# Kernel optimization log

Hardware: AMD Instinct MI355X
Metric: run time of the kernel (lower is better)

Reference implementation:

```python
import jax, jax.numpy as jnp
import numpy as np
import math

B, T, C = 8, 2048, 1024
N_LAYER, LAYER_ID = 24, 12


def setup_inputs() -> dict:
    key = jax.random.key(0)
    ks = jax.random.split(key, 8)
    # deterministic parameter init, mirroring RWKV_TimeMix.__init__
    ratio_0_to_1 = LAYER_ID / (N_LAYER - 1)
    ratio_1_to_almost0 = 1.0 - LAYER_ID / N_LAYER
    h = np.arange(C, dtype=np.float64)
    time_decay = (-5 + 8 * (h / (C - 1)) ** (0.7 + 1.3 * ratio_0_to_1)).astype(np.float32)
    zigzag = (np.array([(i + 1) % 3 - 1 for i in range(C)], dtype=np.float64) * 0.5)
    time_first = (np.ones(C) * math.log(0.3) + zigzag).astype(np.float32)
    xpos = (np.arange(C, dtype=np.float64) / C)
    time_mix_k = (xpos ** ratio_1_to_almost0).astype(np.float32).reshape(1, 1, C)
    time_mix_v = (xpos ** ratio_1_to_almost0 + 0.3 * ratio_0_to_1).astype(np.float32).reshape(1, 1, C)
    time_mix_r = (xpos ** (0.5 * ratio_1_to_almost0)).astype(np.float32).reshape(1, 1, C)
    scale = 1.0 / math.sqrt(C)
    return {
        "x": jax.random.normal(ks[0], (B, T, C), jnp.float32),
        "time_decay": jnp.asarray(time_decay),
        "time_first": jnp.asarray(time_first),
        "time_mix_k": jnp.asarray(time_mix_k),
        "time_mix_v": jnp.asarray(time_mix_v),
        "time_mix_r": jnp.asarray(time_mix_r),
        "Wk": jax.random.normal(ks[1], (C, C), jnp.float32) * scale,
        "Wv": jax.random.normal(ks[2], (C, C), jnp.float32) * scale,
        "Wr": jax.random.normal(ks[3], (C, C), jnp.float32) * scale,
        "Wo": jax.random.normal(ks[4], (C, C), jnp.float32) * scale,
    }


def wkv_scan(w_decay, u, k, v):
    """Numerically-stable RWKV-4 WKV recurrence.
    w_decay, u: [C]; k, v: [B, T, C]. Returns [B, T, C].
    """
    w = -jnp.exp(w_decay)  # negative decay per channel
    kt = jnp.swapaxes(k, 0, 1)  # [T, B, C]
    vt = jnp.swapaxes(v, 0, 1)
    Bn, Cn = k.shape[0], k.shape[2]
    aa0 = jnp.zeros((Bn, Cn), k.dtype)
    bb0 = jnp.zeros((Bn, Cn), k.dtype)
    pp0 = jnp.full((Bn, Cn), -1e38, k.dtype)

    def step(carry, kv):
        aa, bb, pp = carry
        k_t, v_t = kv
        ww = u + k_t
        q = jnp.maximum(pp, ww)
        e1 = jnp.exp(pp - q)
        e2 = jnp.exp(ww - q)
        y = (e1 * aa + e2 * v_t) / (e1 * bb + e2)
        ww2 = pp + w
        q2 = jnp.maximum(ww2, k_t)
        e1 = jnp.exp(ww2 - q2)
        e2 = jnp.exp(k_t - q2)
        return (e1 * aa + e2 * v_t, e1 * bb + e2, q2), y

    _, ys = jax.lax.scan(step, (aa0, bb0, pp0), (kt, vt))
    return jnp.swapaxes(ys, 0, 1)  # [B, T, C]


def reference(x, time_decay, time_first, time_mix_k, time_mix_v, time_mix_r, Wk, Wv, Wr, Wo):
    # time shift: x_{t-1}, zero at t=0
    xx = jnp.pad(x, ((0, 0), (1, 0), (0, 0)))[:, :-1]
    xk = x * time_mix_k + xx * (1.0 - time_mix_k)
    xv = x * time_mix_v + xx * (1.0 - time_mix_v)
    xr = x * time_mix_r + xx * (1.0 - time_mix_r)
    k = jnp.einsum("btc,oc->bto", xk, Wk)
    v = jnp.einsum("btc,oc->bto", xv, Wv)
    r = jnp.einsum("btc,oc->bto", xr, Wr)
    wkv = wkv_scan(time_decay, time_first, k, v)
    rwkv = jax.nn.sigmoid(r) * wkv
    return jnp.einsum("btc,oc->bto", rwkv, Wo)
```

## Files before the change

kernel.cpp:

```cpp
#include <hip/hip_runtime.h>

#define BB 8
#define TT 2048
#define CC 1024
#define WKV_L 64
#define WKV_NCH (TT / WKV_L)

typedef __bf16 bf16x8_t __attribute__((ext_vector_type(8)));
typedef float f32x4_t __attribute__((ext_vector_type(4)));

__device__ __forceinline__ unsigned short f2bf(float f) {
  unsigned u = __float_as_uint(f);
  u += 0x7fffu + ((u >> 16) & 1u);
  return (unsigned short)(u >> 16);
}
__device__ __forceinline__ float bf2f(unsigned short s) {
  return __uint_as_float(((unsigned)s) << 16);
}

#define GLOAD16(gp, lp)                                                        \
  __builtin_amdgcn_global_load_lds(                                            \
      (const __attribute__((address_space(1))) void*)(gp),                     \
      (__attribute__((address_space(3))) void*)(lp), 16, 0, 0)

__global__ __launch_bounds__(256) void mix3_cast_kernel(
    const float* __restrict__ x, const float* __restrict__ tmk,
    const float* __restrict__ tmv, const float* __restrict__ tmr,
    unsigned short* __restrict__ xk, unsigned short* __restrict__ xv,
    unsigned short* __restrict__ xr) {
  const size_t total4 = (size_t)BB * TT * CC / 4;
  for (size_t i = (size_t)blockIdx.x * blockDim.x + threadIdx.x; i < total4;
       i += (size_t)gridDim.x * blockDim.x) {
    size_t e = i * 4;
    int c = (int)(e & (CC - 1));
    int t = (int)((e / CC) & (TT - 1));
    float4 xv4 = ((const float4*)x)[i];
    float4 xp = make_float4(0.f, 0.f, 0.f, 0.f);
    if (t > 0) xp = ((const float4*)x)[i - CC / 4];
    float4 mk = *(const float4*)(tmk + c);
    float4 mv = *(const float4*)(tmv + c);
    float4 mr = *(const float4*)(tmr + c);
    ushort4 ok, ov, orr;
    ok.x = f2bf(xv4.x * mk.x + xp.x * (1.f - mk.x));
    ok.y = f2bf(xv4.y * mk.y + xp.y * (1.f - mk.y));
    ok.z = f2bf(xv4.z * mk.z + xp.z * (1.f - mk.z));
    ok.w = f2bf(xv4.w * mk.w + xp.w * (1.f - mk.w));
    ov.x = f2bf(xv4.x * mv.x + xp.x * (1.f - mv.x));
    ov.y = f2bf(xv4.y * mv.y + xp.y * (1.f - mv.y));
    ov.z = f2bf(xv4.z * mv.z + xp.z * (1.f - mv.z));
    ov.w = f2bf(xv4.w * mv.w + xp.w * (1.f - mv.w));
    orr.x = f2bf(xv4.x * mr.x + xp.x * (1.f - mr.x));
    orr.y = f2bf(xv4.y * mr.y + xp.y * (1.f - mr.y));
    orr.z = f2bf(xv4.z * mr.z + xp.z * (1.f - mr.z));
    orr.w = f2bf(xv4.w * mr.w + xp.w * (1.f - mr.w));
    *(ushort4*)(xk + e) = ok;
    *(ushort4*)(xv + e) = ov;
    *(ushort4*)(xr + e) = orr;
  }
}

__global__ __launch_bounds__(256) void mix_cast_kernel(const float* __restrict__ x,
                                const float* __restrict__ tmix,
                                unsigned short* __restrict__ out) {
  const size_t total4 = (size_t)BB * TT * CC / 4;
  for (size_t i = (size_t)blockIdx.x * blockDim.x + threadIdx.x; i < total4;
       i += (size_t)gridDim.x * blockDim.x) {
    size_t e = i * 4;
    int c = (int)(e & (CC - 1));
    int t = (int)((e / CC) & (TT - 1));
    float4 xv = ((const float4*)x)[i];
    float4 xp = make_float4(0.f, 0.f, 0.f, 0.f);
    if (t > 0) xp = ((const float4*)x)[i - CC / 4];
    float4 tm = *(const float4*)(tmix + c);
    ushort4 o;
    o.x = f2bf(xv.x * tm.x + xp.x * (1.f - tm.x));
    o.y = f2bf(xv.y * tm.y + xp.y * (1.f - tm.y));
    o.z = f2bf(xv.z * tm.z + xp.z * (1.f - tm.z));
    o.w = f2bf(xv.w * tm.w + xp.w * (1.f - tm.w));
    *(ushort4*)(out + e) = o;
  }
}

__global__ __launch_bounds__(256) void cast_w4_kernel(
    const float* __restrict__ w0, const float* __restrict__ w1,
    const float* __restrict__ w2, const float* __restrict__ w3,
    unsigned short* __restrict__ o0, unsigned short* __restrict__ o1,
    unsigned short* __restrict__ o2, unsigned short* __restrict__ o3) {
  const int n4 = CC * CC / 4;
  for (int i = blockIdx.x * blockDim.x + threadIdx.x; i < 4 * n4;
       i += gridDim.x * blockDim.x) {
    int sel = i / n4;
    int j = i - sel * n4;
    const float* w = sel == 0 ? w0 : sel == 1 ? w1 : sel == 2 ? w2 : w3;
    unsigned short* o = sel == 0 ? o0 : sel == 1 ? o1 : sel == 2 ? o2 : o3;
    float4 v = ((const float4*)w)[j];
    ushort4 u;
    u.x = f2bf(v.x); u.y = f2bf(v.y); u.z = f2bf(v.z); u.w = f2bf(v.w);
    ((ushort4*)o)[j] = u;
  }
}

#define NT8 (CC / 64)

template <typename EPI>
__device__ __forceinline__ void gemm8_body(unsigned short* lds8,
                                           const unsigned short* __restrict__ A,
                                           const unsigned short* __restrict__ Bm,
                                           int tm, int tn, EPI epi) {
  const int tid = threadIdx.x;
  const int lane = tid & 63;
  const int wid = tid >> 6;
  const int wr = wid >> 2;
  const int wc = wid & 3;
  const int fr = lane & 15;
  const int fk = lane >> 4;

  const int srow = tid >> 3;
  const int gcol = (((tid & 7) ^ (srow & 7)) << 3);
  const unsigned short* Ag = A + (size_t)(tm * 256 + srow) * CC + gcol;
  const unsigned short* Bg = Bm + (size_t)(tn * 256 + srow) * CC + gcol;
  const int ldst = tid << 3;

  const int rowA = wr * 16 + fr;
  const int rowB = wc * 16 + fr;
  const int sx0 = ((fk ^ (fr & 7)) << 3);
  const int sx1 = (((4 + fk) ^ (fr & 7)) << 3);

  bf16x8_t aF[4][2];
  bf16x8_t bF[2][2][2];
  f32x4_t acc[8][4] = {};

#define STG_A(T, H)                                                            \
  {                                                                            \
    const unsigned short* g_ = Ag + (size_t)((H) * 128) * CC + (T) * 64;       \
    unsigned short* l_ = &lds8[(((T) & 1) << 14) + (H) * 8192 + ldst];         \
    GLOAD16(g_, l_);                                                           \
    GLOAD16(g_ + (size_t)64 * CC, l_ + 4096);                                  \
  }
#define STG_B(T, H)                                                            \
  {                                                                            \
    const unsigned short* g_ = Bg + (size_t)((H) * 128) * CC + (T) * 64;       \
    unsigned short* l_ = &lds8[32768 + (((T) & 1) << 14) + (H) * 8192 + ldst]; \
    GLOAD16(g_, l_);                                                           \
    GLOAD16(g_ + (size_t)64 * CC, l_ + 4096);                                  \
  }
#define LOADA(MH)                                                              \
  _Pragma("unroll") for (int i_ = 0; i_ < 4; ++i_) {                           \
    aF[i_][0] = *(const bf16x8_t*)&lds8[ab + ((MH) * 4 + i_) * 2048 + sx0];    \
    aF[i_][1] = *(const bf16x8_t*)&lds8[ab + ((MH) * 4 + i_) * 2048 + sx1];    \
  }
#define LOADB(NH)                                                              \
  _Pragma("unroll") for (int j_ = 0; j_ < 2; ++j_) {                           \
    bF[NH][j_][0] = *(const bf16x8_t*)&lds8[bb + ((NH) * 2 + j_) * 4096 + sx0];\
    bF[NH][j_][1] = *(const bf16x8_t*)&lds8[bb + ((NH) * 2 + j_) * 4096 + sx1];\
  }
#define MFMAQ(MH, NH)                                                          \
  _Pragma("unroll") for (int i_ = 0; i_ < 4; ++i_)                             \
  _Pragma("unroll") for (int j_ = 0; j_ < 2; ++j_) {                           \
    acc[(MH) * 4 + i_][(NH) * 2 + j_] = __builtin_amdgcn_mfma_f32_16x16x32_bf16( \
        aF[i_][0], bF[NH][j_][0], acc[(MH) * 4 + i_][(NH) * 2 + j_], 0, 0, 0); \
    acc[(MH) * 4 + i_][(NH) * 2 + j_] = __builtin_amdgcn_mfma_f32_16x16x32_bf16( \
        aF[i_][1], bF[NH][j_][1], acc[(MH) * 4 + i_][(NH) * 2 + j_], 0, 0, 0); \
  }

  STG_A(0, 0) STG_B(0, 0) STG_A(0, 1) STG_B(0, 1)
  STG_A(1, 0) STG_B(1, 0) STG_A(1, 1)
  asm volatile("s_waitcnt vmcnt(10)" ::: "memory");
  __builtin_amdgcn_s_barrier();

  for (int t = 0; t < NT8; ++t) {
    const int ab = ((t & 1) << 14) + rowA * 64;
    const int bb = 32768 + ((t & 1) << 14) + rowB * 64;
    LOADA(0) LOADB(0)
    if (t + 1 < NT8) { STG_B(t + 1, 1) }
    asm volatile("s_waitcnt vmcnt(8)" ::: "memory");
    __builtin_amdgcn_s_barrier();
    __builtin_amdgcn_s_setprio(1);
    MFMAQ(0, 0)
    __builtin_amdgcn_s_setprio(0);
    __builtin_amdgcn_s_barrier();
    LOADB(1)
    if (t + 2 < NT8) { STG_A(t + 2, 0) }
    __builtin_amdgcn_s_barrier();
    __builtin_amdgcn_s_setprio(1);
    MFMAQ(0, 1)
    __builtin_amdgcn_s_setprio(0);
    __builtin_amdgcn_s_barrier();
    LOADA(1)
    if (t + 2 < NT8) { STG_B(t + 2, 0) }
    __builtin_amdgcn_s_barrier();
    __builtin_amdgcn_s_setprio(1);
    MFMAQ(1, 0)
    __builtin_amdgcn_s_setprio(0);
    __builtin_amdgcn_s_barrier();
    if (t + 2 < NT8) { STG_A(t + 2, 1) }
    asm volatile("s_waitcnt vmcnt(10)" ::: "memory");
    __builtin_amdgcn_s_barrier();
    __builtin_amdgcn_s_setprio(1);
    MFMAQ(1, 1)
    __builtin_amdgcn_s_setprio(0);
    __builtin_amdgcn_s_barrier();
  }

#pragma unroll
  for (int im = 0; im < 8; ++im)
#pragma unroll
    for (int jn = 0; jn < 4; ++jn)
#pragma unroll
      for (int rg = 0; rg < 4; ++rg)
        epi((size_t)(tm * 256 + wr * 16 + im * 32 + (fk << 2) + rg) * CC +
                (size_t)(tn * 256 + wc * 16 + jn * 64 + fr),
            acc[im][jn][rg]);
#undef STG_A
#undef STG_B
#undef LOADA
#undef LOADB
#undef MFMAQ
}

__global__ __launch_bounds__(512, 2) void gemm8_kvr(
    const unsigned short* __restrict__ xk, const unsigned short* __restrict__ xv,
    const unsigned short* __restrict__ xr, const unsigned short* __restrict__ Wk,
    const unsigned short* __restrict__ Wv, const unsigned short* __restrict__ Wr,
    float* __restrict__ kout, unsigned short* __restrict__ vout,
    unsigned short* __restrict__ rout) {
  __shared__ unsigned short lds8[65536];
  int orig = blockIdx.x;
  int wg = (orig & 7) * 96 + (orig >> 3);
  int which = wg >> 8;
  int rr = wg & 255;
  int tm = rr >> 2;
  int tn = rr & 3;
  if (which == 0) {
    gemm8_body(lds8, xk, Wk, tm, tn,
               [&](size_t off, float val) { kout[off] = val; });
  } else {
    const unsigned short* A = which == 1 ? xv : xr;
    const unsigned short* Bm = which == 1 ? Wv : Wr;
    unsigned short* o = which == 1 ? vout : rout;
    gemm8_body(lds8, A, Bm, tm, tn,
               [&](size_t off, float val) { o[off] = f2bf(val); });
  }
}

template <int OUT_BF16>
__global__ __launch_bounds__(512, 2) void gemm8_one(const unsigned short* __restrict__ A,
                         const unsigned short* __restrict__ Bm,
                         void* __restrict__ Cm) {
  __shared__ unsigned short lds8[65536];
  int orig = blockIdx.x;
  int wg = (orig & 7) * 32 + (orig >> 3);
  int tm = wg >> 2;
  int tn = wg & 3;
  if (OUT_BF16)
    gemm8_body(lds8, A, Bm, tm, tn,
               [&](size_t off, float val) { ((unsigned short*)Cm)[off] = f2bf(val); });
  else
    gemm8_body(lds8, A, Bm, tm, tn,
               [&](size_t off, float val) { ((float*)Cm)[off] = val; });
}

__global__ __launch_bounds__(256) void wkv_phase1(const float* __restrict__ k,
                           const unsigned short* __restrict__ v,
                           const float* __restrict__ wdec,
                           float* __restrict__ Sa, float* __restrict__ Sb,
                           float* __restrict__ Sp) {
  int idx = blockIdx.x * blockDim.x + threadIdx.x;
  int c = idx & (CC - 1);
  int bj = idx >> 10;
  int j = bj % WKV_NCH;
  int b = bj / WKV_NCH;
  float w = -__expf(wdec[c]);
  size_t base = (size_t)b * TT * CC + (size_t)j * WKV_L * CC + c;
  float aa = 0.f, bb = 0.f, pp = -1e38f;
  for (int t = 0; t < WKV_L; ++t) {
    size_t off = base + (size_t)t * CC;
    float kt = k[off];
    float vt = bf2f(v[off]);
    float ww2 = pp + w;
    float q2 = fmaxf(ww2, kt);
    float f1 = __expf(ww2 - q2);
    float f2 = __expf(kt - q2);
    aa = fmaf(f1, aa, f2 * vt);
    bb = fmaf(f1, bb, f2);
    pp = q2;
  }
  Sa[idx] = aa; Sb[idx] = bb; Sp[idx] = pp;
}

__global__ __launch_bounds__(256) void wkv_phase2(const float* __restrict__ wdec,
                           const float* __restrict__ Sa, const float* __restrict__ Sb,
                           const float* __restrict__ Sp,
                           float* __restrict__ Ia, float* __restrict__ Ib,
                           float* __restrict__ Ip) {
  int idx = blockIdx.x * blockDim.x + threadIdx.x;
  if (idx >= BB * CC) return;
  int c = idx & (CC - 1);
  int b = idx >> 10;
  float wL = -__expf(wdec[c]) * (float)WKV_L;
  float aa = 0.f, bb = 0.f, pp = -1e38f;
  for (int j = 0; j < WKV_NCH; ++j) {
    size_t s = (size_t)(b * WKV_NCH + j) * CC + c;
    Ia[s] = aa; Ib[s] = bb; Ip[s] = pp;
    float pd = pp + wL;
    float ps = Sp[s];
    float q = fmaxf(pd, ps);
    float e1 = __expf(pd - q);
    float e2 = __expf(ps - q);
    aa = fmaf(e1, aa, e2 * Sa[s]);
    bb = fmaf(e1, bb, e2 * Sb[s]);
    pp = q;
  }
}

__global__ __launch_bounds__(256) void wkv_phase3(const float* __restrict__ k,
                           const unsigned short* __restrict__ v,
                           const unsigned short* __restrict__ r,
                           const float* __restrict__ wdec,
                           const float* __restrict__ u,
                           const float* __restrict__ Ia, const float* __restrict__ Ib,
                           const float* __restrict__ Ip,
                           unsigned short* __restrict__ out) {
  int idx = blockIdx.x * blockDim.x + threadIdx.x;
  int c = idx & (CC - 1);
  int bj = idx >> 10;
  int j = bj % WKV_NCH;
  int b = bj / WKV_NCH;
  float w = -__expf(wdec[c]);
  float uu = u[c];
  float aa = Ia[idx], bb = Ib[idx], pp = Ip[idx];
  size_t base = (size_t)b * TT * CC + (size_t)j * WKV_L * CC + c;
  for (int t = 0; t < WKV_L; ++t) {
    size_t off = base + (size_t)t * CC;
    float kt = k[off];
    float vt = bf2f(v[off]);
    float ww = uu + kt;
    float q = fmaxf(pp, ww);
    float e1 = __expf(pp - q);
    float e2 = __expf(ww - q);
    float y = fmaf(e1, aa, e2 * vt) / fmaf(e1, bb, e2);
    float ww2 = pp + w;
    float q2 = fmaxf(ww2, kt);
    float f1 = __expf(ww2 - q2);
    float f2 = __expf(kt - q2);
    aa = fmaf(f1, aa, f2 * vt);
    bb = fmaf(f1, bb, f2);
    pp = q2;
    float rt = bf2f(r[off]);
    float sr = 1.f / (1.f + __expf(-rt));
    out[off] = f2bf(sr * y);
  }
}

extern "C" void kernel_launch(void* const* d_in, const int* in_sizes, int n_in,
                              void* d_out, int out_size, void* d_ws, size_t ws_size,
                              hipStream_t stream) {
  const float* x    = (const float*)d_in[0];
  const float* tdec = (const float*)d_in[1];
  const float* tfir = (const float*)d_in[2];
  const float* tmk  = (const float*)d_in[3];
  const float* tmv  = (const float*)d_in[4];
  const float* tmr  = (const float*)d_in[5];
  const float* Wk   = (const float*)d_in[6];
  const float* Wv   = (const float*)d_in[7];
  const float* Wr   = (const float*)d_in[8];
  const float* Wo   = (const float*)d_in[9];

  const size_t M = (size_t)BB * TT;
  const size_t mixbytes = M * CC * 2;
  const size_t wbytes = (size_t)CC * CC * 2;
  const size_t nstate = (size_t)BB * WKV_NCH * CC;

  const size_t need_big = 3 * mixbytes + 4 * wbytes + (M * CC * 4) + 2 * mixbytes +
                          mixbytes + 6 * nstate * 4;
  const bool big = ws_size >= need_big;

  char* ws = (char*)d_ws;
  unsigned short* xkb = (unsigned short*)ws; ws += mixbytes;
  unsigned short* xvb = xkb, *xrb = xkb;
  if (big) {
    xvb = (unsigned short*)ws; ws += mixbytes;
    xrb = (unsigned short*)ws; ws += mixbytes;
  }
  unsigned short* Wkb = (unsigned short*)ws; ws += wbytes;
  unsigned short* Wvb = (unsigned short*)ws; ws += wbytes;
  unsigned short* Wrb = (unsigned short*)ws; ws += wbytes;
  unsigned short* Wob = (unsigned short*)ws; ws += wbytes;
  float* kbuf = (float*)ws;                   ws += M * CC * 4;
  unsigned short* vbuf = (unsigned short*)ws; ws += mixbytes;
  unsigned short* rbuf = (unsigned short*)ws; ws += mixbytes;
  float* Sa = (float*)ws; ws += nstate * 4;
  float* Sb = (float*)ws; ws += nstate * 4;
  float* Sp = (float*)ws; ws += nstate * 4;
  float* Ia = (float*)ws; ws += nstate * 4;
  float* Ib = (float*)ws; ws += nstate * 4;
  float* Ip = (float*)ws; ws += nstate * 4;

  dim3 blk(256);
  dim3 blk8(512);
  const int wkv_grid = (int)(nstate / 256);

  cast_w4_kernel<<<1024, blk, 0, stream>>>(Wk, Wv, Wr, Wo, Wkb, Wvb, Wrb, Wob);

  if (big) {
    mix3_cast_kernel<<<2048, blk, 0, stream>>>(x, tmk, tmv, tmr, xkb, xvb, xrb);
    gemm8_kvr<<<768, blk8, 0, stream>>>(xkb, xvb, xrb, Wkb, Wvb, Wrb,
                                        kbuf, vbuf, rbuf);
  } else {
    mix_cast_kernel<<<2048, blk, 0, stream>>>(x, tmk, xkb);
    gemm8_one<0><<<256, blk8, 0, stream>>>(xkb, Wkb, kbuf);
    mix_cast_kernel<<<2048, blk, 0, stream>>>(x, tmv, xkb);
    gemm8_one<1><<<256, blk8, 0, stream>>>(xkb, Wvb, vbuf);
    mix_cast_kernel<<<2048, blk, 0, stream>>>(x, tmr, xkb);
    gemm8_one<1><<<256, blk8, 0, stream>>>(xkb, Wrb, rbuf);
  }

  wkv_phase1<<<wkv_grid, blk, 0, stream>>>(kbuf, vbuf, tdec, Sa, Sb, Sp);
  wkv_phase2<<<(BB * CC + 255) / 256, blk, 0, stream>>>(tdec, Sa, Sb, Sp, Ia, Ib, Ip);
  wkv_phase3<<<wkv_grid, blk, 0, stream>>>(kbuf, vbuf, rbuf, tdec, tfir, Ia, Ib, Ip, xkb);

  gemm8_one<0><<<256, blk8, 0, stream>>>(xkb, Wob, d_out);
}
```

Baseline: 291.7 us.

## Replace fused KVR GEMM launch with separate GEMMs and reuse buffers to shrink workspace

Drops the single 768-block K/V/R GEMM launch and the ws_size-dependent path. It now mixes K and V in one pass, runs three 256-block GEMMs, mixes R separately, and aliases R's buffer onto the V-mix buffer. wkv_phase3 writes its output in place over r, so __restrict__ is removed from those pointers. The GEMM main loop also gets #pragma unroll. This cuts workspace and memory footprint but adds launches and a second read pass over x, and loses the concurrency of one 768-block grid.

```diff
diff --git a/kernel.cpp b/kernel.cpp
--- a/kernel.cpp
+++ b/kernel.cpp
@@ -23,11 +23,10 @@
       (const __attribute__((address_space(1))) void*)(gp),                     \
       (__attribute__((address_space(3))) void*)(lp), 16, 0, 0)
 
-__global__ __launch_bounds__(256) void mix3_cast_kernel(
+__global__ __launch_bounds__(256) void mix2_cast_kernel(
     const float* __restrict__ x, const float* __restrict__ tmk,
-    const float* __restrict__ tmv, const float* __restrict__ tmr,
-    unsigned short* __restrict__ xk, unsigned short* __restrict__ xv,
-    unsigned short* __restrict__ xr) {
+    const float* __restrict__ tmv,
+    unsigned short* __restrict__ xk, unsigned short* __restrict__ xv) {
   const size_t total4 = (size_t)BB * TT * CC / 4;
   for (size_t i = (size_t)blockIdx.x * blockDim.x + threadIdx.x; i < total4;
        i += (size_t)gridDim.x * blockDim.x) {
@@ -39,8 +38,7 @@
     if (t > 0) xp = ((const float4*)x)[i - CC / 4];
     float4 mk = *(const float4*)(tmk + c);
     float4 mv = *(const float4*)(tmv + c);
-    float4 mr = *(const float4*)(tmr + c);
-    ushort4 ok, ov, orr;
+    ushort4 ok, ov;
     ok.x = f2bf(xv4.x * mk.x + xp.x * (1.f - mk.x));
     ok.y = f2bf(xv4.y * mk.y + xp.y * (1.f - mk.y));
     ok.z = f2bf(xv4.z * mk.z + xp.z * (1.f - mk.z));
@@ -49,13 +47,8 @@
     ov.y = f2bf(xv4.y * mv.y + xp.y * (1.f - mv.y));
     ov.z = f2bf(xv4.z * mv.z + xp.z * (1.f - mv.z));
     ov.w = f2bf(xv4.w * mv.w + xp.w * (1.f - mv.w));
-    orr.x = f2bf(xv4.x * mr.x + xp.x * (1.f - mr.x));
-    orr.y = f2bf(xv4.y * mr.y + xp.y * (1.f - mr.y));
-    orr.z = f2bf(xv4.z * mr.z + xp.z * (1.f - mr.z));
-    orr.w = f2bf(xv4.w * mr.w + xp.w * (1.f - mr.w));
     *(ushort4*)(xk + e) = ok;
     *(ushort4*)(xv + e) = ov;
-    *(ushort4*)(xr + e) = orr;
   }
 }
 
@@ -168,6 +161,7 @@
   asm volatile("s_waitcnt vmcnt(10)" ::: "memory");
   __builtin_amdgcn_s_barrier();
 
+#pragma unroll
   for (int t = 0; t < NT8; ++t) {
     const int ab = ((t & 1) << 14) + rowA * 64;
     const int bb = 32768 + ((t & 1) << 14) + rowB * 64;
@@ -216,31 +210,6 @@
 #undef LOADA
 #undef LOADB
 #undef MFMAQ
-}
-
-__global__ __launch_bounds__(512, 2) void gemm8_kvr(
-    const unsigned short* __restrict__ xk, const unsigned short* __restrict__ xv,
-    const unsigned short* __restrict__ xr, const unsigned short* __restrict__ Wk,
-    const unsigned short* __restrict__ Wv, const unsigned short* __restrict__ Wr,
-    float* __restrict__ kout, unsigned short* __restrict__ vout,
-    unsigned short* __restrict__ rout) {
-  __shared__ unsigned short lds8[65536];
-  int orig = blockIdx.x;
-  int wg = (orig & 7) * 96 + (orig >> 3);
-  int which = wg >> 8;
-  int rr = wg & 255;
-  int tm = rr >> 2;
-  int tn = rr & 3;
-  if (which == 0) {
-    gemm8_body(lds8, xk, Wk, tm, tn,
-               [&](size_t off, float val) { kout[off] = val; });
-  } else {
-    const unsigned short* A = which == 1 ? xv : xr;
-    const unsigned short* Bm = which == 1 ? Wv : Wr;
-    unsigned short* o = which == 1 ? vout : rout;
-    gemm8_body(lds8, A, Bm, tm, tn,
-               [&](size_t off, float val) { o[off] = f2bf(val); });
-  }
 }
 
 template <int OUT_BF16>
@@ -315,12 +284,12 @@
 
 __global__ __launch_bounds__(256) void wkv_phase3(const float* __restrict__ k,
                            const unsigned short* __restrict__ v,
-                           const unsigned short* __restrict__ r,
+                           const unsigned short* r,
                            const float* __restrict__ wdec,
                            const float* __restrict__ u,
                            const float* __restrict__ Ia, const float* __restrict__ Ib,
                            const float* __restrict__ Ip,
-                           unsigned short* __restrict__ out) {
+                           unsigned short* out) {
   int idx = blockIdx.x * blockDim.x + threadIdx.x;
   int c = idx & (CC - 1);
   int bj = idx >> 10;
@@ -371,24 +340,16 @@
   const size_t wbytes = (size_t)CC * CC * 2;
   const size_t nstate = (size_t)BB * WKV_NCH * CC;
 
-  const size_t need_big = 3 * mixbytes + 4 * wbytes + (M * CC * 4) + 2 * mixbytes +
-                          mixbytes + 6 * nstate * 4;
-  const bool big = ws_size >= need_big;
-
   char* ws = (char*)d_ws;
-  unsigned short* xkb = (unsigned short*)ws; ws += mixbytes;
-  unsigned short* xvb = xkb, *xrb = xkb;
-  if (big) {
-    xvb = (unsigned short*)ws; ws += mixbytes;
-    xrb = (unsigned short*)ws; ws += mixbytes;
-  }
+  unsigned short* xkb = (unsigned short*)ws;  ws += mixbytes;
+  unsigned short* xvb = (unsigned short*)ws;  ws += mixbytes;
+  unsigned short* rbuf = xvb;
   unsigned short* Wkb = (unsigned short*)ws; ws += wbytes;
   unsigned short* Wvb = (unsigned short*)ws; ws += wbytes;
   unsigned short* Wrb = (unsigned short*)ws; ws += wbytes;
   unsigned short* Wob = (unsigned short*)ws; ws += wbytes;
   float* kbuf = (float*)ws;                   ws += M * CC * 4;
   unsigned short* vbuf = (unsigned short*)ws; ws += mixbytes;
-  unsigned short* rbuf = (unsigned short*)ws; ws += mixbytes;
   float* Sa = (float*)ws; ws += nstate * 4;
   float* Sb = (float*)ws; ws += nstate * 4;
   float* Sp = (float*)ws; ws += nstate * 4;
@@ -401,23 +362,16 @@
   const int wkv_grid = (int)(nstate / 256);
 
   cast_w4_kernel<<<1024, blk, 0, stream>>>(Wk, Wv, Wr, Wo, Wkb, Wvb, Wrb, Wob);
-
-  if (big) {
-    mix3_cast_kernel<<<2048, blk, 0, stream>>>(x, tmk, tmv, tmr, xkb, xvb, xrb);
-    gemm8_kvr<<<768, blk8, 0, stream>>>(xkb, xvb, xrb, Wkb, Wvb, Wrb,
-                                        kbuf, vbuf, rbuf);
-  } else {
-    mix_cast_kernel<<<2048, blk, 0, stream>>>(x, tmk, xkb);
-    gemm8_one<0><<<256, blk8, 0, stream>>>(xkb, Wkb, kbuf);
-    mix_cast_kernel<<<2048, blk, 0, stream>>>(x, tmv, xkb);
-    gemm8_one<1><<<256, blk8, 0, stream>>>(xkb, Wvb, vbuf);
-    mix_cast_kernel<<<2048, blk, 0, stream>>>(x, tmr, xkb);
-    gemm8_one<1><<<256, blk8, 0, stream>>>(xkb, Wrb, rbuf);
-  }
+  mix2_cast_kernel<<<2048, blk, 0, stream>>>(x, tmk, tmv, xkb, xvb);
+  gemm8_one<0><<<256, blk8, 0, stream>>>(xkb, Wkb, kbuf);
+  gemm8_one<1><<<256, blk8, 0, stream>>>(xvb, Wvb, vbuf);
+  mix_cast_kernel<<<2048, blk, 0, stream>>>(x, tmr, xkb);
+  gemm8_one<1><<<256, blk8, 0, stream>>>(xkb, Wrb, rbuf);
 
   wkv_phase1<<<wkv_grid, blk, 0, stream>>>(kbuf, vbuf, tdec, Sa, Sb, Sp);
   wkv_phase2<<<(BB * CC + 255) / 256, blk, 0, stream>>>(tdec, Sa, Sb, Sp, Ia, Ib, Ip);
-  wkv_phase3<<<wkv_grid, blk, 0, stream>>>(kbuf, vbuf, rbuf, tdec, tfir, Ia, Ib, Ip, xkb);
-
-  gemm8_one<0><<<256, blk8, 0, stream>>>(xkb, Wob, d_out);
-}
+  wkv_phase3<<<wkv_grid, blk, 0, stream>>>(kbuf, vbuf, rbuf, tdec, tfir,
+                                           Ia, Ib, Ip, rbuf);
+
+  gemm8_one<0><<<256, blk8, 0, stream>>>(rbuf, Wob, d_out);
+}
```

After: 273.9 us. -6.1%, faster.
